# Kernel tuning notes

Measured on AMD Instinct MI355X. Metric: run time of the kernel, lower is better.

Reference implementation:

```python
import jax, jax.numpy as jnp
import numpy as np

N_NODES = 100_000
N_EDGES = 1_600_000
F_DIM = 32


def setup_inputs() -> dict:
    key = jax.random.key(0)
    k1, k2, k3 = jax.random.split(key, 3)
    x = jax.random.normal(k1, (N_NODES, F_DIM), dtype=jnp.float32)
    edge_index = jax.random.randint(k2, (2, N_EDGES), 0, N_NODES, dtype=jnp.int64)
    edge_weight = jax.random.uniform(k3, (N_EDGES,), dtype=jnp.float32)
    w_mp = jnp.array([0.5], dtype=jnp.float32)  # learned scalar parameter
    return {"x": x, "edge_index": edge_index, "edge_weight": edge_weight, "w_mp": w_mp}


def reference(x, edge_index, edge_weight, w_mp):
    # message: ea = w_mp * x[src] * edge_weight  (shape [E, F])
    # aggregate: sum messages into target nodes (aggr='add', source_to_target)
    src = edge_index[0]
    dst = edge_index[1]
    ea = (w_mp * x[src]) * edge_weight[:, None]          # [E, F]
    out = jax.ops.segment_sum(ea, dst, num_segments=x.shape[0])  # [N, F]
    return out
```

## Files before the change

### kernel.cpp

```cpp
#include <hip/hip_runtime.h>


constexpr int N_NODES = 100000;
constexpr int N_EDGES = 1600000;
constexpr int F_DIM   = 32;

constexpr int NPB = 256;
constexpr int NB  = (N_NODES + NPB - 1) / NPB;
constexpr int CAP = 4608;

constexpr int BIN_THREADS = 512;
constexpr int BIN_EPT     = 16;
constexpr int BIN_CHUNK   = BIN_THREADS * BIN_EPT;
constexpr int BIN_BLOCKS  = (N_EDGES + BIN_CHUNK - 1) / BIN_CHUNK;

constexpr int SORT_THREADS = 512;
constexpr int RPT = (CAP + SORT_THREADS - 1) / SORT_THREADS;

constexpr size_t WS_CURSOR  = 0;
constexpr size_t WS_BEGIN   = 4096;
constexpr size_t WS_END     = WS_BEGIN + 400000;
constexpr size_t WS_RECORDS = WS_END + 400000;
constexpr size_t WS_NEEDED  = WS_RECORDS + (size_t)NB * CAP * 8;

__global__ __launch_bounds__(256) void init_cursors(int* __restrict__ gcursor)
{
    int i = blockIdx.x * 256 + threadIdx.x;
    if (i < NB) gcursor[i] = i * CAP;
}

__global__ __launch_bounds__(BIN_THREADS) void bin_edges(
    const int* __restrict__ src, const int* __restrict__ dst,
    const float* __restrict__ ew, const float* __restrict__ w_mp,
    int* __restrict__ gcursor, uint2* __restrict__ records)
{
    __shared__ int lhist[NB];
    __shared__ int lbase[NB];
    for (int i = threadIdx.x; i < NB; i += BIN_THREADS) lhist[i] = 0;
    __syncthreads();

    const float w = w_mp[0];
    const int base_e = blockIdx.x * BIN_CHUNK;
    int   bkt[BIN_EPT];
    uint2 rec[BIN_EPT];

    #pragma unroll
    for (int i = 0; i < BIN_EPT; ++i) {
        int e = base_e + threadIdx.x + i * BIN_THREADS;
        bkt[i] = -1;
        if (e < N_EDGES) {
            int d = dst[e];
            int b = d >> 8;
            bkt[i] = b;
            rec[i].x = __float_as_uint(w * ew[e]);
            rec[i].y = (unsigned)src[e] | ((unsigned)(d & 255) << 24);
            atomicAdd(&lhist[b], 1);
        }
    }
    __syncthreads();

    for (int i = threadIdx.x; i < NB; i += BIN_THREADS) {
        int c = lhist[i];
        lbase[i] = c ? atomicAdd(&gcursor[i], c) : 0;
        lhist[i] = 0;
    }
    __syncthreads();

    #pragma unroll
    for (int i = 0; i < BIN_EPT; ++i) {
        int b = bkt[i];
        if (b >= 0) {
            int pos = lbase[b] + atomicAdd(&lhist[b], 1);
            if (pos < (b + 1) * CAP)
                records[pos] = rec[i];
        }
    }
}

__global__ __launch_bounds__(SORT_THREADS) void bucket_sort(
    const int* __restrict__ gcursor, uint2* __restrict__ records,
    int* __restrict__ begin, int* __restrict__ end)
{
    __shared__ uint2 sorted[CAP];
    __shared__ int   scan[NPB + 1];
    __shared__ int   cursor[NPB];

    const int b     = blockIdx.x;
    const int t     = threadIdx.x;
    const int rbase = b * CAP;
    int cnt = min(gcursor[b] - rbase, CAP);

    if (t <= NPB) scan[t] = 0;
    if (t < NPB)  cursor[t] = 0;
    __syncthreads();

    uint2 rec[RPT];
    bool  have[RPT];
    #pragma unroll
    for (int i = 0; i < RPT; ++i) {
        int j = t + i * SORT_THREADS;
        have[i] = (j < cnt);
        if (have[i]) {
            rec[i] = records[rbase + j];
            atomicAdd(&cursor[rec[i].y >> 24], 1);
        }
    }
    __syncthreads();

    if (t < NPB) scan[t + 1] = cursor[t];
    __syncthreads();
    for (int d = 1; d < NPB; d <<= 1) {
        int v = 0;
        if (t >= 1 && t <= NPB) v = (t > d) ? scan[t - d] : 0;
        __syncthreads();
        if (t >= 1 && t <= NPB) scan[t] += v;
        __syncthreads();
    }
    if (t < NPB) cursor[t] = scan[t];
    __syncthreads();

    #pragma unroll
    for (int i = 0; i < RPT; ++i) {
        if (have[i]) {
            int slot = atomicAdd(&cursor[rec[i].y >> 24], 1);
            sorted[slot] = rec[i];
        }
    }
    __syncthreads();

    #pragma unroll
    for (int i = 0; i < RPT; ++i) {
        int j = t + i * SORT_THREADS;
        if (j < cnt) records[rbase + j] = sorted[j];
    }

    int node0 = b * NPB;
    if (t < NPB && node0 + t < N_NODES) {
        begin[node0 + t] = rbase + scan[t];
        end[node0 + t]   = rbase + scan[t + 1];
    }
}

__global__ __launch_bounds__(256) void gather(
    const int* __restrict__ begin, const int* __restrict__ end,
    const uint2* __restrict__ records, const float* __restrict__ x,
    float* __restrict__ out)
{
    int gid  = blockIdx.x * 256 + threadIdx.x;
    int node = gid >> 3;
    int q    = (gid & 7) * 4;
    if (node >= N_NODES) return;

    int j  = begin[node];
    int je = end[node];
    float4 acc = make_float4(0.f, 0.f, 0.f, 0.f);
    for (; j < je; ++j) {
        uint2 r = records[j];
        float c = __uint_as_float(r.x);
        int   s = r.y & 0xFFFFFF;
        const float4 xv = *reinterpret_cast<const float4*>(
            x + (size_t)s * F_DIM + q);
        acc.x += c * xv.x;
        acc.y += c * xv.y;
        acc.z += c * xv.z;
        acc.w += c * xv.w;
    }
    *reinterpret_cast<float4*>(out + (size_t)node * F_DIM + q) = acc;
}

__global__ __launch_bounds__(256) void gnn_scatter_atomic(
    const float* __restrict__ x, const int* __restrict__ src,
    const int* __restrict__ dst, const float* __restrict__ ew,
    const float* __restrict__ w_mp, float* __restrict__ out)
{
    const float w = w_mp[0];
    int gid = blockIdx.x * blockDim.x + threadIdx.x;
    int e = gid >> 3;
    int qq = (gid & 7) * 4;
    if (e >= N_EDGES) return;
    int s = src[e];
    int d = dst[e];
    float c = w * ew[e];
    const float4 xv = *reinterpret_cast<const float4*>(x + (size_t)s * F_DIM + qq);
    float* op = out + (size_t)d * F_DIM + qq;
    atomicAdd(op + 0, c * xv.x);
    atomicAdd(op + 1, c * xv.y);
    atomicAdd(op + 2, c * xv.z);
    atomicAdd(op + 3, c * xv.w);
}

extern "C" void kernel_launch(void* const* d_in, const int* in_sizes, int n_in,
                              void* d_out, int out_size, void* d_ws, size_t ws_size,
                              hipStream_t stream) {
    const float* x    = (const float*)d_in[0];
    const int*   ei   = (const int*)d_in[1];
    const float* ew   = (const float*)d_in[2];
    const float* w_mp = (const float*)d_in[3];
    float* out = (float*)d_out;

    const int* src = ei;
    const int* dst = ei + N_EDGES;

    if (ws_size < WS_NEEDED) {
        hipMemsetAsync(d_out, 0, (size_t)out_size * sizeof(float), stream);
        int total = N_EDGES * 8;
        gnn_scatter_atomic<<<(total + 255) / 256, 256, 0, stream>>>(
            x, src, dst, ew, w_mp, out);
        return;
    }

    char* ws = (char*)d_ws;
    int*   gcursor = (int*)(ws + WS_CURSOR);
    int*   begin   = (int*)(ws + WS_BEGIN);
    int*   end     = (int*)(ws + WS_END);
    uint2* records = (uint2*)(ws + WS_RECORDS);

    init_cursors<<<(NB + 255) / 256, 256, 0, stream>>>(gcursor);
    bin_edges<<<BIN_BLOCKS, BIN_THREADS, 0, stream>>>(src, dst, ew, w_mp,
                                                      gcursor, records);
    bucket_sort<<<NB, SORT_THREADS, 0, stream>>>(gcursor, records, begin, end);

    int gthreads = N_NODES * 8;
    gather<<<(gthreads + 255) / 256, 256, 0, stream>>>(begin, end, records, x, out);
}
```

Measured before the change: 142.4 us.

## Fuse bucket sort with gather into one kernel using 64-node buckets

Merges the bucket_sort and gather kernels, so each block sorts its bucket's records in shared memory and then accumulates straight from that sorted LDS array. This removes the write-back of sorted records to global memory, the begin/end index arrays, their global re-reads and one kernel launch. Buckets shrink from 256 to 64 nodes so one 512-thread block can cover 8 threads per node. The prefix scan becomes a single-wavefront shuffle scan, and the gather loop is unrolled by four to keep more loads in flight. In exchange, binning now tracks about four times as many buckets per block, which means more shared-memory histogram entries and more global cursor atomics per binning block.

```diff
diff --git a/kernel.cpp b/kernel.cpp
--- a/kernel.cpp
+++ b/kernel.cpp
@@ -5,22 +5,20 @@
 constexpr int N_EDGES = 1600000;
 constexpr int F_DIM   = 32;
 
-constexpr int NPB = 256;
+constexpr int NPB = 64;
 constexpr int NB  = (N_NODES + NPB - 1) / NPB;
-constexpr int CAP = 4608;
+constexpr int CAP = 1344;
 
 constexpr int BIN_THREADS = 512;
-constexpr int BIN_EPT     = 16;
+constexpr int BIN_EPT     = 8;
 constexpr int BIN_CHUNK   = BIN_THREADS * BIN_EPT;
 constexpr int BIN_BLOCKS  = (N_EDGES + BIN_CHUNK - 1) / BIN_CHUNK;
 
-constexpr int SORT_THREADS = 512;
-constexpr int RPT = (CAP + SORT_THREADS - 1) / SORT_THREADS;
+constexpr int AGG_THREADS = 512;
+constexpr int RPT = (CAP + AGG_THREADS - 1) / AGG_THREADS;
 
 constexpr size_t WS_CURSOR  = 0;
-constexpr size_t WS_BEGIN   = 4096;
-constexpr size_t WS_END     = WS_BEGIN + 400000;
-constexpr size_t WS_RECORDS = WS_END + 400000;
+constexpr size_t WS_RECORDS = 8192;
 constexpr size_t WS_NEEDED  = WS_RECORDS + (size_t)NB * CAP * 8;
 
 __global__ __launch_bounds__(256) void init_cursors(int* __restrict__ gcursor)
@@ -50,10 +48,10 @@
         bkt[i] = -1;
         if (e < N_EDGES) {
             int d = dst[e];
-            int b = d >> 8;
+            int b = d >> 6;
             bkt[i] = b;
             rec[i].x = __float_as_uint(w * ew[e]);
-            rec[i].y = (unsigned)src[e] | ((unsigned)(d & 255) << 24);
+            rec[i].y = (unsigned)src[e] | ((unsigned)(d & 63) << 24);
             atomicAdd(&lhist[b], 1);
         }
     }
@@ -77,95 +75,101 @@
     }
 }
 
-__global__ __launch_bounds__(SORT_THREADS) void bucket_sort(
-    const int* __restrict__ gcursor, uint2* __restrict__ records,
-    int* __restrict__ begin, int* __restrict__ end)
+__global__ __launch_bounds__(AGG_THREADS) void sort_gather(
+    const int*   __restrict__ gcursor,
+    const uint2* __restrict__ records,
+    const float* __restrict__ x,
+    float*       __restrict__ out)
 {
     __shared__ uint2 sorted[CAP];
-    __shared__ int   scan[NPB + 1];
+    __shared__ int   hist[NPB];
+    __shared__ int   offs[NPB + 1];
     __shared__ int   cursor[NPB];
 
     const int b     = blockIdx.x;
     const int t     = threadIdx.x;
     const int rbase = b * CAP;
-    int cnt = min(gcursor[b] - rbase, CAP);
-
-    if (t <= NPB) scan[t] = 0;
-    if (t < NPB)  cursor[t] = 0;
+    const int cnt   = min(gcursor[b] - rbase, CAP);
+
+    if (t < NPB) hist[t] = 0;
     __syncthreads();
 
     uint2 rec[RPT];
-    bool  have[RPT];
     #pragma unroll
     for (int i = 0; i < RPT; ++i) {
-        int j = t + i * SORT_THREADS;
-        have[i] = (j < cnt);
-        if (have[i]) {
+        int j = t + i * AGG_THREADS;
+        rec[i].y = 0xFFFFFFFFu;
+        if (j < cnt) {
             rec[i] = records[rbase + j];
-            atomicAdd(&cursor[rec[i].y >> 24], 1);
-        }
-    }
-    __syncthreads();
-
-    if (t < NPB) scan[t + 1] = cursor[t];
-    __syncthreads();
-    for (int d = 1; d < NPB; d <<= 1) {
-        int v = 0;
-        if (t >= 1 && t <= NPB) v = (t > d) ? scan[t - d] : 0;
-        __syncthreads();
-        if (t >= 1 && t <= NPB) scan[t] += v;
-        __syncthreads();
-    }
-    if (t < NPB) cursor[t] = scan[t];
+            atomicAdd(&hist[rec[i].y >> 24], 1);
+        }
+    }
+    __syncthreads();
+
+    if (t < 64) {
+        int v   = hist[t];
+        int inc = v;
+        #pragma unroll
+        for (int d = 1; d < 64; d <<= 1) {
+            int o = __shfl_up(inc, d, 64);
+            if (t >= d) inc += o;
+        }
+        offs[t + 1] = inc;
+        if (t == 0) offs[0] = 0;
+        cursor[t] = inc - v;
+    }
     __syncthreads();
 
     #pragma unroll
     for (int i = 0; i < RPT; ++i) {
-        if (have[i]) {
-            int slot = atomicAdd(&cursor[rec[i].y >> 24], 1);
+        if (rec[i].y != 0xFFFFFFFFu) {
+            int dl   = rec[i].y >> 24;
+            int slot = atomicAdd(&cursor[dl], 1);
             sorted[slot] = rec[i];
         }
     }
     __syncthreads();
 
-    #pragma unroll
-    for (int i = 0; i < RPT; ++i) {
-        int j = t + i * SORT_THREADS;
-        if (j < cnt) records[rbase + j] = sorted[j];
-    }
-
-    int node0 = b * NPB;
-    if (t < NPB && node0 + t < N_NODES) {
-        begin[node0 + t] = rbase + scan[t];
-        end[node0 + t]   = rbase + scan[t + 1];
-    }
-}
-
-__global__ __launch_bounds__(256) void gather(
-    const int* __restrict__ begin, const int* __restrict__ end,
-    const uint2* __restrict__ records, const float* __restrict__ x,
-    float* __restrict__ out)
-{
-    int gid  = blockIdx.x * 256 + threadIdx.x;
-    int node = gid >> 3;
-    int q    = (gid & 7) * 4;
-    if (node >= N_NODES) return;
-
-    int j  = begin[node];
-    int je = end[node];
+    const int node  = t >> 3;
+    const int q     = (t & 7) * 4;
+    const int gnode = b * NPB + node;
+    if (gnode >= N_NODES) return;
+
+    int j  = offs[node];
+    int je = offs[node + 1];
     float4 acc = make_float4(0.f, 0.f, 0.f, 0.f);
+
+    for (; j + 4 <= je; j += 4) {
+        uint2 r0 = sorted[j + 0];
+        uint2 r1 = sorted[j + 1];
+        uint2 r2 = sorted[j + 2];
+        uint2 r3 = sorted[j + 3];
+        const float4 v0 = *reinterpret_cast<const float4*>(
+            x + (size_t)(r0.y & 0xFFFFFFu) * F_DIM + q);
+        const float4 v1 = *reinterpret_cast<const float4*>(
+            x + (size_t)(r1.y & 0xFFFFFFu) * F_DIM + q);
+        const float4 v2 = *reinterpret_cast<const float4*>(
+            x + (size_t)(r2.y & 0xFFFFFFu) * F_DIM + q);
+        const float4 v3 = *reinterpret_cast<const float4*>(
+            x + (size_t)(r3.y & 0xFFFFFFu) * F_DIM + q);
+        float c0 = __uint_as_float(r0.x), c1 = __uint_as_float(r1.x);
+        float c2 = __uint_as_float(r2.x), c3 = __uint_as_float(r3.x);
+        acc.x += c0 * v0.x + c1 * v1.x + c2 * v2.x + c3 * v3.x;
+        acc.y += c0 * v0.y + c1 * v1.y + c2 * v2.y + c3 * v3.y;
+        acc.z += c0 * v0.z + c1 * v1.z + c2 * v2.z + c3 * v3.z;
+        acc.w += c0 * v0.w + c1 * v1.w + c2 * v2.w + c3 * v3.w;
+    }
     for (; j < je; ++j) {
-        uint2 r = records[j];
+        uint2 r = sorted[j];
         float c = __uint_as_float(r.x);
-        int   s = r.y & 0xFFFFFF;
-        const float4 xv = *reinterpret_cast<const float4*>(
-            x + (size_t)s * F_DIM + q);
-        acc.x += c * xv.x;
-        acc.y += c * xv.y;
-        acc.z += c * xv.z;
-        acc.w += c * xv.w;
-    }
-    *reinterpret_cast<float4*>(out + (size_t)node * F_DIM + q) = acc;
+        const float4 v = *reinterpret_cast<const float4*>(
+            x + (size_t)(r.y & 0xFFFFFFu) * F_DIM + q);
+        acc.x += c * v.x;
+        acc.y += c * v.y;
+        acc.z += c * v.z;
+        acc.w += c * v.w;
+    }
+    *reinterpret_cast<float4*>(out + (size_t)gnode * F_DIM + q) = acc;
 }
 
 __global__ __launch_bounds__(256) void gnn_scatter_atomic(
@@ -211,15 +215,10 @@
 
     char* ws = (char*)d_ws;
     int*   gcursor = (int*)(ws + WS_CURSOR);
-    int*   begin   = (int*)(ws + WS_BEGIN);
-    int*   end     = (int*)(ws + WS_END);
     uint2* records = (uint2*)(ws + WS_RECORDS);
 
     init_cursors<<<(NB + 255) / 256, 256, 0, stream>>>(gcursor);
     bin_edges<<<BIN_BLOCKS, BIN_THREADS, 0, stream>>>(src, dst, ew, w_mp,
                                                       gcursor, records);
-    bucket_sort<<<NB, SORT_THREADS, 0, stream>>>(gcursor, records, begin, end);
-
-    int gthreads = N_NODES * 8;
-    gather<<<(gthreads + 255) / 256, 256, 0, stream>>>(begin, end, records, x, out);
-}
+    sort_gather<<<NB, AGG_THREADS, 0, stream>>>(gcursor, records, x, out);
+}
```

Measured after the change: 135.9 us. 4.5% less time.
